# Kernel optimization log

Hardware: AMD Instinct MI355X
Metric: run time of the kernel (lower is better)

Reference implementation:

```python
import jax, jax.numpy as jnp
import numpy as np

B, D, N, H = 2, 1024, 2048, 16
DH = D // H  # head dim 64


def setup_inputs() -> dict:
    key = jax.random.key(0)
    ks = jax.random.split(key, 10)
    query = jax.random.normal(ks[0], (B, D, N), jnp.float32)
    att_mask = jax.random.randint(ks[1], (B, 1, N), 0, 2).astype(bool)
    w = lambda k: jax.random.normal(k, (D, D), jnp.float32) * 0.02
    b = lambda k: jax.random.normal(k, (D,), jnp.float32) * 0.02
    return dict(
        query=query,
        Wq=w(ks[2]), bq=b(ks[3]),
        Wk=w(ks[4]), bk=b(ks[5]),
        Wv=w(ks[6]), bv=b(ks[7]),
        Wo=w(ks[8]), bo=b(ks[9]),
        att_mask=att_mask,
    )


def _proj(W, bias, x):  # conv1d k=1: [B,D,N] -> [B,D,N]
    return jnp.einsum('ed,bdn->ben', W, x) + bias[None, :, None]


def _split_heads(t):  # [B,N,D] -> [B*H,N,DH], batch-major flatten
    return t.reshape(B, N, H, DH).transpose(0, 2, 1, 3).reshape(B * H, N, DH)


def _attention(q, k, v, att_mask):
    scale = 1.0 / np.sqrt(DH)
    att = jnp.einsum('bqd,bkd->bqk', q * scale, k)  # [B*H,N,N]
    # faithful to original: mask repeated along q_len then tiled num_heads times on dim 0
    m = jnp.tile(jnp.broadcast_to(att_mask, (B, N, N)), (H, 1, 1))
    att = jnp.where(m, att, -jnp.inf)
    fully_masked = ~m.any(axis=(-2, -1))  # [B*H]
    att = jnp.where(fully_masked[:, None, None], 1e-5, att)
    p = jax.nn.softmax(att, axis=-1)
    y = jnp.einsum('bqk,bkd->bqd', p, v)
    return y * (~fully_masked).astype(y.dtype)[:, None, None]


def reference(query, Wq, bq, Wk, bk, Wv, bv, Wo, bo, att_mask):
    # projections (Conv1d kernel_size=1 == channel-dim linear)
    q = _split_heads(_proj(Wq, bq, query).transpose(0, 2, 1))
    k = _split_heads(_proj(Wk, bk, query).transpose(0, 2, 1))
    v = _split_heads(_proj(Wv, bv, query).transpose(0, 2, 1))
    y = _attention(q, k, v, att_mask)  # [B*H,N,DH]
    # combine heads -> [B,N,D] -> channels-first [B,D,N]
    z = y.reshape(B, H, N, DH).transpose(0, 2, 1, 3).reshape(B, N, D).transpose(0, 2, 1)
    # output projection (dropouts are identity in eval mode)
    return _proj(Wo, bo, z)
```

## Files before the change

### kernel.cpp

```cpp
#include <hip/hip_runtime.h>
#include <hip/hip_bf16.h>

#define BATCH 2
#define DMODEL 1024
#define SEQ 2048
#define NHEAD 16
#define DHEAD 64
#define BH (BATCH*NHEAD)
#define COLS (BATCH*SEQ)

typedef __attribute__((ext_vector_type(8))) short bf16x8;
typedef __attribute__((ext_vector_type(4))) float f32x4;
typedef __attribute__((ext_vector_type(16))) float f32x16;

__device__ inline unsigned short f2bf(float f) {
    unsigned u = __builtin_bit_cast(unsigned, f);
    unsigned r = (u + 0x7FFFu + ((u >> 16) & 1u)) >> 16;
    return (unsigned short)r;
}

__device__ inline f32x4 mfma16(bf16x8 a, bf16x8 b, f32x4 c) {
    return __builtin_amdgcn_mfma_f32_16x16x32_bf16(a, b, c, 0, 0, 0);
}
__device__ inline f32x16 mfma32(bf16x8 a, bf16x8 b, f32x16 c) {
    return __builtin_amdgcn_mfma_f32_32x32x16_bf16(a, b, c, 0, 0, 0);
}

__device__ __forceinline__ void gload_lds16(const unsigned short* g, unsigned short* l) {
    __builtin_amdgcn_global_load_lds(
        (const __attribute__((address_space(1))) unsigned int*)g,
        (__attribute__((address_space(3))) unsigned int*)l, 16, 0, 0);
}

__device__ inline unsigned cvtpk(float lo, float hi) {
    unsigned r;
    asm("v_cvt_pk_bf16_f32 %0, %1, %2" : "=v"(r) : "v"(lo), "v"(hi));
    return r;
}
__device__ inline float fexp2(float x) {
    float r;
    asm("v_exp_f32 %0, %1" : "=v"(r) : "v"(x));
    return r;
}

__global__ __launch_bounds__(256) void cvt_w(
    const float* __restrict__ w0, const float* __restrict__ w1,
    const float* __restrict__ w2, const float* __restrict__ w3,
    unsigned short* __restrict__ out)
{
    int which = blockIdx.y;
    const float* src = (which == 0) ? w0 : (which == 1) ? w1 : (which == 2) ? w2 : w3;
    size_t base = (size_t)which * (DMODEL * DMODEL);
    size_t i = ((size_t)blockIdx.x * 256 + threadIdx.x) * 4;
    float4 v = *(const float4*)&src[i];
    ushort4 o;
    o.x = f2bf(v.x); o.y = f2bf(v.y); o.z = f2bf(v.z); o.w = f2bf(v.w);
    *(ushort4*)&out[base + i] = o;
}

__global__ __launch_bounds__(64) void prep_mask(
    const int* __restrict__ mask, unsigned long long* __restrict__ mw,
    unsigned short* __restrict__ maskvb)
{
    int lane = threadIdx.x;
    int tile = blockIdx.x;
    int mb = tile >> 5, tt = tile & 31;
    int mv = mask[mb * SEQ + tt * 64 + lane];
    unsigned long long bits = __ballot(mv != 0);
    if (lane == 0) mw[tile] = bits;
    int q2 = (lane >> 2) & 3;
    int q2s = ((q2 & 1) << 1) | (q2 >> 1);
    int pp = (lane & ~15) | (q2s << 2) | (lane & 3);
    maskvb[mb * SEQ + tt * 64 + pp] = mv ? 0x3F80 : 0;
}

__global__ __launch_bounds__(256) void transpose_q(
    const float* __restrict__ q, unsigned short* __restrict__ Xt)
{
    __shared__ float tile[32][33];
    int b = blockIdx.z;
    int d0 = blockIdx.y * 32, n0 = blockIdx.x * 32;
    int tx = threadIdx.x, ty = threadIdx.y;
#pragma unroll
    for (int i = 0; i < 32; i += 8)
        tile[ty + i][tx] = q[(size_t)b * DMODEL * SEQ + (size_t)(d0 + ty + i) * SEQ + n0 + tx];
    __syncthreads();
#pragma unroll
    for (int i = 0; i < 32; i += 8)
        Xt[(size_t)b * SEQ * DMODEL + (size_t)(n0 + ty + i) * DMODEL + d0 + tx] = f2bf(tile[tx][ty + i]);
}

__global__ __launch_bounds__(256) void gemm_qkv(
    const unsigned short* __restrict__ Xt,
    const unsigned short* __restrict__ W3,
    const float* __restrict__ bq, const float* __restrict__ bk, const float* __restrict__ bv,
    const int* __restrict__ mask,
    unsigned short* __restrict__ Qb, unsigned short* __restrict__ Kbuf,
    unsigned short* __restrict__ Vtb)
{
    const int K = DMODEL;
    __shared__ unsigned short sA[128 * 32];
    __shared__ unsigned short sB[128 * 32];
    int t = threadIdx.x, lane = t & 63, w = t >> 6;
    int wr = w >> 1, wc = w & 1;
    int tt0 = blockIdx.y * 128;
    int ct0 = blockIdx.x * 128;
    int mat = ct0 >> 10, ec0 = ct0 & 1023;
    const float* bs = (mat == 0) ? bq : (mat == 1) ? bk : bv;
    int rl = lane & 15, ko = (lane >> 4) << 3;
    int srow = lane >> 2, scol = (lane & 3) << 3;

    f32x4 acc[4][4] = {};
    for (int kb = 0; kb < K; kb += 32) {
        __syncthreads();
        gload_lds16(&Xt[(size_t)(tt0 + w * 32 + srow) * K + kb + scol],      &sA[(w * 32) * 32]);
        gload_lds16(&Xt[(size_t)(tt0 + w * 32 + 16 + srow) * K + kb + scol], &sA[(w * 32 + 16) * 32]);
        gload_lds16(&W3[(size_t)(ct0 + w * 32 + srow) * K + kb + scol],      &sB[(w * 32) * 32]);
        gload_lds16(&W3[(size_t)(ct0 + w * 32 + 16 + srow) * K + kb + scol], &sB[(w * 32 + 16) * 32]);
        __syncthreads();
        bf16x8 af[4], bfr[4];
#pragma unroll
        for (int m = 0; m < 4; m++)
            af[m] = *(const bf16x8*)&sA[(wr * 64 + m * 16 + rl) * 32 + ko];
#pragma unroll
        for (int n = 0; n < 4; n++)
            bfr[n] = *(const bf16x8*)&sB[(wc * 64 + n * 16 + rl) * 32 + ko];
#pragma unroll
        for (int m = 0; m < 4; m++)
#pragma unroll
            for (int n = 0; n < 4; n++)
                acc[m][n] = mfma16(af[m], bfr[n], acc[m][n]);
    }

    const float QS = 0.125f;
    int rowb = (lane >> 4) * 4, col = lane & 15;
#pragma unroll
    for (int m = 0; m < 4; m++) {
#pragma unroll
        for (int n = 0; n < 4; n++) {
            int ee = ec0 + wc * 64 + n * 16 + col;
            int hh = ee >> 6, dd = ee & 63;
            float bias = bs[ee];
#pragma unroll
            for (int r = 0; r < 4; r++) {
                int tk = tt0 + wr * 64 + m * 16 + rowb + r;
                int b = tk >> 11, nn = tk & (SEQ - 1);
                float v = acc[m][n][r] + bias;
                if (mat == 0) {
                    v *= QS;
                    Qb[((size_t)(b * NHEAD + hh) * SEQ + nn) * DHEAD + dd] = f2bf(v);
                } else if (mat == 1) {
                    Kbuf[((size_t)(b * NHEAD + hh) * SEQ + nn) * DHEAD + dd] = f2bf(v);
                } else {
                    if (mask[(hh & 1) * SEQ + nn] == 0) v = 0.f;
                    int q2 = (nn >> 2) & 3;
                    int q2s = ((q2 & 1) << 1) | (q2 >> 1);
                    int np = (nn & ~15) | (q2s << 2) | (nn & 3);
                    int tl = np >> 6, kk = np & 63;
                    int ks = kk >> 4, hi2 = (kk >> 3) & 1, jj = kk & 7;
                    Vtb[((((size_t)(b * NHEAD + hh) * 32 + tl) * 8 + ks * 2 + hi2) * 64 + dd) * 8 + jj] = f2bf(v);
                }
            }
        }
    }
}

__global__ __launch_bounds__(256) void gemm_out(
    const unsigned short* __restrict__ A,
    const unsigned short* __restrict__ Bt,
    const float* __restrict__ bias,
    float* __restrict__ outf)
{
    const int K = DMODEL;
    __shared__ unsigned short sA[128 * 32];
    __shared__ unsigned short sB[64 * 32];
    int t = threadIdx.x, lane = t & 63, w = t >> 6;
    int wr = w >> 1, wc = w & 1;
    int et0 = blockIdx.y * 128, ct0 = blockIdx.x * 64;
    int rl = lane & 15, ko = (lane >> 4) << 3;
    int srow = lane >> 2, scol = (lane & 3) << 3;

    f32x4 acc[4][2] = {};
    for (int kb = 0; kb < K; kb += 32) {
        __syncthreads();
        gload_lds16(&A[(size_t)(et0 + w * 16 + srow) * K + kb + scol],      &sA[(w * 16) * 32]);
        gload_lds16(&A[(size_t)(et0 + 64 + w * 16 + srow) * K + kb + scol], &sA[(64 + w * 16) * 32]);
        gload_lds16(&Bt[(size_t)(ct0 + w * 16 + srow) * K + kb + scol],     &sB[(w * 16) * 32]);
        __syncthreads();
        bf16x8 af[4], bfr[2];
#pragma unroll
        for (int m = 0; m < 4; m++)
            af[m] = *(const bf16x8*)&sA[(wr * 64 + m * 16 + rl) * 32 + ko];
#pragma unroll
        for (int n = 0; n < 2; n++)
            bfr[n] = *(const bf16x8*)&sB[(wc * 32 + n * 16 + rl) * 32 + ko];
#pragma unroll
        for (int m = 0; m < 4; m++)
#pragma unroll
            for (int n = 0; n < 2; n++)
                acc[m][n] = mfma16(af[m], bfr[n], acc[m][n]);
    }

    int rowb = (lane >> 4) * 4, col = lane & 15;
#pragma unroll
    for (int m = 0; m < 4; m++) {
#pragma unroll
        for (int n = 0; n < 2; n++) {
            int c = ct0 + wc * 32 + n * 16 + col;
            int b = c >> 11, nn = c & (SEQ - 1);
#pragma unroll
            for (int r = 0; r < 4; r++) {
                int e = et0 + wr * 64 + m * 16 + rowb + r;
                outf[((size_t)b * DMODEL + e) * SEQ + nn] = acc[m][n][r] + bias[e];
            }
        }
    }
}

__global__ __launch_bounds__(256, 2) void attn(
    const unsigned short* __restrict__ Q,
    const unsigned short* __restrict__ Kb,
    const unsigned short* __restrict__ Vt,
    const unsigned long long* __restrict__ mwords,
    const unsigned short* __restrict__ maskvb,
    unsigned short* __restrict__ Zt)
{
    __shared__ unsigned short sK[2][64 * 64];

    int bid = blockIdx.x;
    int xcd = bid & 7, slot = bid >> 3;
    int bh = xcd + 8 * (slot >> 4);
    int qb = slot & 15;
    int b = bh >> 4, h = bh & 15;
    int mb = bh & (BATCH - 1);
    int t = threadIdx.x, lane = t & 63, w = t >> 6;
    int hi = lane >> 5, ql = lane & 31;
    int q0 = qb * 128 + w * 32;
    const unsigned short* Qp = Q + (size_t)bh * SEQ * DHEAD;
    const unsigned short* Kp = Kb + (size_t)bh * SEQ * DHEAD;
    const unsigned short* Vg = Vt + (size_t)bh * SEQ * DHEAD;
    const unsigned long long* mw = mwords + mb * 32;
    const unsigned short* Mv = maskvb + mb * SEQ;

    int srow0 = w * 16 + (lane >> 3);
    int ssw   = ((lane & 7) ^ ((lane >> 3) & 7)) << 3;

    unsigned long long anyb = 0ull;
#pragma unroll
    for (int i = 0; i < 32; i++) anyb |= mw[i];

    bf16x8 qf[4];
#pragma unroll
    for (int c = 0; c < 4; c++)
        qf[c] = *(const bf16x8*)&Qp[(size_t)(q0 + ql) * DHEAD + c * 16 + hi * 8];

    f32x16 Y0 = {}, Y1 = {}, Yl = {};
    float m_ = -1e30f;
    const float LOG2E = 1.442695041f;

    int rsw = ql & 7;

    gload_lds16(&Kp[(size_t)srow0 * DHEAD + ssw],       &sK[0][(w * 16) * 64]);
    gload_lds16(&Kp[(size_t)(srow0 + 8) * DHEAD + ssw], &sK[0][(w * 16 + 8) * 64]);
    __syncthreads();

    for (int tt0 = 0; tt0 < 32; tt0++) {
        int cur = tt0 & 1;
        if (tt0 < 31) {
            int kn = (tt0 + 1) * 64;
            gload_lds16(&Kp[(size_t)(kn + srow0) * DHEAD + ssw],     &sK[cur ^ 1][(w * 16) * 64]);
            gload_lds16(&Kp[(size_t)(kn + srow0 + 8) * DHEAD + ssw], &sK[cur ^ 1][(w * 16 + 8) * 64]);
        }

        const unsigned short* vt = &Vg[(size_t)tt0 * 4096];
        bf16x8 vb0[4], vb1[4], im[4];
#pragma unroll
        for (int ks = 0; ks < 4; ks++) {
            vb0[ks] = *(const bf16x8*)&vt[(size_t)((ks * 2 + hi) * 64 + ql) * 8];
            vb1[ks] = *(const bf16x8*)&vt[(size_t)((ks * 2 + hi) * 64 + 32 + ql) * 8];
            im[ks]  = *(const bf16x8*)&Mv[tt0 * 64 + 16 * ks + 8 * hi];
        }

        f32x16 S0 = {}, S1 = {};
        __builtin_amdgcn_s_setprio(1);
#pragma unroll
        for (int c = 0; c < 4; c++) {
            bf16x8 kf = *(const bf16x8*)&sK[cur][ql * 64 + ((((c << 1) | hi) ^ rsw) << 3)];
            S0 = mfma32(kf, qf[c], S0);
        }
#pragma unroll
        for (int c = 0; c < 4; c++) {
            bf16x8 kf = *(const bf16x8*)&sK[cur][(32 + ql) * 64 + ((((c << 1) | hi) ^ rsw) << 3)];
            S1 = mfma32(kf, qf[c], S1);
        }
        __builtin_amdgcn_s_setprio(0);

        float t0[16];
#pragma unroll
        for (int r = 0; r < 16; r++) t0[r] = fmaxf(S0[r], S1[r]);
#pragma unroll
        for (int s = 8; s > 0; s >>= 1)
#pragma unroll
            for (int r = 0; r < 8; r++)
                if (r < s) t0[r] = fmaxf(t0[r], t0[r + s]);

        if (!__all(t0[0] <= m_ + 8.0f)) {
            float pmax = fmaxf(t0[0], __shfl_xor(t0[0], 32, 64));
            float mnew = fmaxf(m_, pmax);
            float al = __expf(m_ - mnew);
            m_ = mnew;
#pragma unroll
            for (int reg = 0; reg < 16; reg++) {
                float av = __shfl(al, (reg & 3) + 8 * (reg >> 2) + 4 * hi, 64);
                Y0[reg] *= av;
                Y1[reg] *= av;
                Yl[reg] *= av;
            }
        }

        float nmL = -m_ * LOG2E;
        float p[32];
#pragma unroll
        for (int rr = 0; rr < 16; rr++) p[rr] = fexp2(fmaf(S0[rr], LOG2E, nmL));
#pragma unroll
        for (int rr = 0; rr < 16; rr++) p[16 + rr] = fexp2(fmaf(S1[rr], LOG2E, nmL));

        unsigned PKa[8], PKb[8];
#pragma unroll
        for (int i = 0; i < 8; i++) {
            PKa[i] = cvtpk(p[4 * i], p[4 * i + 1]);
            PKb[i] = cvtpk(p[4 * i + 2], p[4 * i + 3]);
        }

        bf16x8 pa[4];
#pragma unroll
        for (int ks = 0; ks < 4; ks++) {
            union { unsigned u[4]; bf16x8 v; } pu;
            pu.u[0] = PKa[2 * ks];
            pu.u[1] = PKb[2 * ks];
            pu.u[2] = PKa[2 * ks + 1];
            pu.u[3] = PKb[2 * ks + 1];
            pa[ks] = pu.v;
        }

        __builtin_amdgcn_s_setprio(1);
#pragma unroll
        for (int ks = 0; ks < 4; ks++) {
            Y0 = mfma32(pa[ks], vb0[ks], Y0);
            Y1 = mfma32(pa[ks], vb1[ks], Y1);
            Yl = mfma32(pa[ks], im[ks],  Yl);
        }
        __builtin_amdgcn_s_setprio(0);

        __syncthreads();
    }

#pragma unroll
    for (int reg = 0; reg < 16; reg++) {
        float lv = (anyb != 0ull) ? (1.0f / Yl[reg]) : 0.f;
        int row = (reg & 3) + 8 * (reg >> 2) + 4 * hi;
        int n = q0 + row;
        size_t base = ((size_t)b * SEQ + n) * DMODEL + h * DHEAD;
        Zt[base + ql] = f2bf(Y0[reg] * lv);
        Zt[base + 32 + ql] = f2bf(Y1[reg] * lv);
    }
}

extern "C" void kernel_launch(void* const* d_in, const int* in_sizes, int n_in,
                              void* d_out, int out_size, void* d_ws, size_t ws_size,
                              hipStream_t stream) {
    const float* query = (const float*)d_in[0];
    const float* Wq = (const float*)d_in[1];
    const float* bq = (const float*)d_in[2];
    const float* Wk = (const float*)d_in[3];
    const float* bk = (const float*)d_in[4];
    const float* Wv = (const float*)d_in[5];
    const float* bv = (const float*)d_in[6];
    const float* Wo = (const float*)d_in[7];
    const float* bo = (const float*)d_in[8];
    const int* mask = (const int*)d_in[9];
    float* out = (float*)d_out;

    char* ws = (char*)d_ws;
    unsigned short* Wb  = (unsigned short*)(ws);
    unsigned short* Xt  = (unsigned short*)(ws + ((size_t)8  << 20));
    unsigned short* Qb  = (unsigned short*)(ws + ((size_t)16 << 20));
    unsigned short* Kbuf= (unsigned short*)(ws + ((size_t)24 << 20));
    unsigned short* Vtb = (unsigned short*)(ws + ((size_t)32 << 20));
    unsigned short* Zt  = (unsigned short*)(ws + ((size_t)40 << 20));
    unsigned long long* mwords = (unsigned long long*)(ws + ((size_t)48 << 20));
    unsigned short* maskvb = (unsigned short*)(ws + ((size_t)48 << 20) + 65536);

    const size_t WSZ = (size_t)DMODEL * DMODEL;

    cvt_w<<<dim3(DMODEL * DMODEL / 1024, 4), 256, 0, stream>>>(Wq, Wk, Wv, Wo, Wb);
    prep_mask<<<64, 64, 0, stream>>>(mask, mwords, maskvb);
    transpose_q<<<dim3(SEQ / 32, DMODEL / 32, BATCH), dim3(32, 8), 0, stream>>>(query, Xt);

    gemm_qkv<<<dim3(3 * DMODEL / 128, COLS / 128), 256, 0, stream>>>(
        Xt, Wb, bq, bk, bv, mask, Qb, Kbuf, Vtb);

    attn<<<512, 256, 0, stream>>>(Qb, Kbuf, Vtb, mwords, maskvb, Zt);

    gemm_out<<<dim3(COLS / 64, DMODEL / 128), 256, 0, stream>>>(
        Wb + 3 * WSZ, Zt, bo, out);
}
```

Baseline: 136.5 us.

## Pre-tile K in projection epilogue and load K fragments directly from global

The projection kernel now writes K in a tiled fragment layout matching the MFMA operand order, like V already is. The attention kernel drops the shared-memory double buffer, the async global-to-LDS copies and the per-tile barrier, and loads K fragments straight from global memory into registers. This removes LDS traffic and block-wide synchronization, but every wave now fetches K separately (relying on L1/L2), and the launch bounds no longer request two blocks per CU.

```diff
diff --git a/kernel.cpp b/kernel.cpp
--- a/kernel.cpp
+++ b/kernel.cpp
@@ -150,7 +150,8 @@
                     v *= QS;
                     Qb[((size_t)(b * NHEAD + hh) * SEQ + nn) * DHEAD + dd] = f2bf(v);
                 } else if (mat == 1) {
-                    Kbuf[((size_t)(b * NHEAD + hh) * SEQ + nn) * DHEAD + dd] = f2bf(v);
+                    int tl = nn >> 6, kk = nn & 63;
+                    Kbuf[((((size_t)(b * NHEAD + hh) * 32 + tl) * 8 + (dd >> 3)) * 64 + kk) * 8 + (dd & 7)] = f2bf(v);
                 } else {
                     if (mask[(hh & 1) * SEQ + nn] == 0) v = 0.f;
                     int q2 = (nn >> 2) & 3;
@@ -217,16 +218,14 @@
     }
 }
 
-__global__ __launch_bounds__(256, 2) void attn(
+__global__ __launch_bounds__(256) void attn(
     const unsigned short* __restrict__ Q,
-    const unsigned short* __restrict__ Kb,
+    const unsigned short* __restrict__ Kg,
     const unsigned short* __restrict__ Vt,
     const unsigned long long* __restrict__ mwords,
     const unsigned short* __restrict__ maskvb,
     unsigned short* __restrict__ Zt)
 {
-    __shared__ unsigned short sK[2][64 * 64];
-
     int bid = blockIdx.x;
     int xcd = bid & 7, slot = bid >> 3;
     int bh = xcd + 8 * (slot >> 4);
@@ -237,14 +236,11 @@
     int hi = lane >> 5, ql = lane & 31;
     int q0 = qb * 128 + w * 32;
     const unsigned short* Qp = Q + (size_t)bh * SEQ * DHEAD;
-    const unsigned short* Kp = Kb + (size_t)bh * SEQ * DHEAD;
+    const unsigned short* Kp = Kg + (size_t)bh * SEQ * DHEAD;
     const unsigned short* Vg = Vt + (size_t)bh * SEQ * DHEAD;
     const unsigned long long* mw = mwords + mb * 32;
     const unsigned short* Mv = maskvb + mb * SEQ;
 
-    int srow0 = w * 16 + (lane >> 3);
-    int ssw   = ((lane & 7) ^ ((lane >> 3) & 7)) << 3;
-
     unsigned long long anyb = 0ull;
 #pragma unroll
     for (int i = 0; i < 32; i++) anyb |= mw[i];
@@ -258,20 +254,14 @@
     float m_ = -1e30f;
     const float LOG2E = 1.442695041f;
 
-    int rsw = ql & 7;
-
-    gload_lds16(&Kp[(size_t)srow0 * DHEAD + ssw],       &sK[0][(w * 16) * 64]);
-    gload_lds16(&Kp[(size_t)(srow0 + 8) * DHEAD + ssw], &sK[0][(w * 16 + 8) * 64]);
-    __syncthreads();
-
     for (int tt0 = 0; tt0 < 32; tt0++) {
-        int cur = tt0 & 1;
-        if (tt0 < 31) {
-            int kn = (tt0 + 1) * 64;
-            gload_lds16(&Kp[(size_t)(kn + srow0) * DHEAD + ssw],     &sK[cur ^ 1][(w * 16) * 64]);
-            gload_lds16(&Kp[(size_t)(kn + srow0 + 8) * DHEAD + ssw], &sK[cur ^ 1][(w * 16 + 8) * 64]);
-        }
-
+        const unsigned short* kt = &Kp[(size_t)tt0 * 4096];
+        bf16x8 kf0[4], kf1[4];
+#pragma unroll
+        for (int c = 0; c < 4; c++) {
+            kf0[c] = *(const bf16x8*)&kt[(size_t)((c * 2 + hi) * 64 + ql) * 8];
+            kf1[c] = *(const bf16x8*)&kt[(size_t)((c * 2 + hi) * 64 + 32 + ql) * 8];
+        }
         const unsigned short* vt = &Vg[(size_t)tt0 * 4096];
         bf16x8 vb0[4], vb1[4], im[4];
 #pragma unroll
@@ -284,15 +274,9 @@
         f32x16 S0 = {}, S1 = {};
         __builtin_amdgcn_s_setprio(1);
 #pragma unroll
-        for (int c = 0; c < 4; c++) {
-            bf16x8 kf = *(const bf16x8*)&sK[cur][ql * 64 + ((((c << 1) | hi) ^ rsw) << 3)];
-            S0 = mfma32(kf, qf[c], S0);
-        }
-#pragma unroll
-        for (int c = 0; c < 4; c++) {
-            bf16x8 kf = *(const bf16x8*)&sK[cur][(32 + ql) * 64 + ((((c << 1) | hi) ^ rsw) << 3)];
-            S1 = mfma32(kf, qf[c], S1);
-        }
+        for (int c = 0; c < 4; c++) S0 = mfma32(kf0[c], qf[c], S0);
+#pragma unroll
+        for (int c = 0; c < 4; c++) S1 = mfma32(kf1[c], qf[c], S1);
         __builtin_amdgcn_s_setprio(0);
 
         float t0[16];
@@ -351,8 +335,6 @@
             Yl = mfma32(pa[ks], im[ks],  Yl);
         }
         __builtin_amdgcn_s_setprio(0);
-
-        __syncthreads();
     }
 
 #pragma unroll
```

Result: slower. 156.8 us (+14.8%).
